# Kernel optimization log

Hardware: AMD Instinct MI355X
Metric: run time of the kernel (lower is better)

Reference implementation:

```python
import jax, jax.numpy as jnp
import numpy as np
from itertools import combinations

NDIM = 256
BATCH = 65536


def setup_inputs() -> dict:
    key = jax.random.key(0)
    k1, k2 = jax.random.split(key)
    pairs = np.array(list(combinations(range(NDIM), 2)), dtype=np.int32)  # [comb(ndim,2), 2]
    return {
        "x": jax.random.normal(k1, (BATCH, NDIM), dtype=jnp.float32),
        "rots": jax.random.normal(k2, (pairs.shape[0],), dtype=jnp.float32),
        "idx_i": jnp.asarray(pairs[:, 0]),
        "idx_j": jnp.asarray(pairs[:, 1]),
    }


def _build_mat(rots, idx_i, idx_j, ndim):
    # Equivalent to mat = R_last @ ... @ R_first @ I, then return mat.T.
    # Each Givens rotation R_(i,j,theta) only mixes rows i and j, so we update
    # two rows per step (O(ndim) work) instead of a dense ndim x ndim matmul.
    # Torch uses cfloat, but all imaginary parts are identically zero, so
    # float32 computes the same math.
    def step(mat, t):
        i, j, theta = t
        c = jnp.cos(theta)
        s = jnp.sin(theta)
        ri = mat[i]
        rj = mat[j]
        mat = mat.at[i].set(c * ri - s * rj)
        mat = mat.at[j].set(s * ri + c * rj)
        return mat, None

    mat0 = jnp.eye(ndim, dtype=rots.dtype)
    mat, _ = jax.lax.scan(step, mat0, (idx_i, idx_j, rots))
    return mat.T  # forward does x @ mat.T


def reference(x, rots, idx_i, idx_j):
    m = _build_mat(rots, idx_i, idx_j, x.shape[-1])  # [ndim, ndim]
    return x @ m
```

## Files before the change

### kernel.cpp

```cpp
#include <hip/hip_runtime.h>
#include <hip/hip_bf16.h>
#include <math.h>

#define NDIM 256
#define NROT 32640
#define NSEG 64
#define SEGLEN 510
#define MATE (NDIM * NDIM)
#define NODEE (2 * MATE)

typedef __bf16 bf16x4_t __attribute__((ext_vector_type(4)));
typedef __bf16 bf16x8_t __attribute__((ext_vector_type(8)));
typedef float f32x4_t __attribute__((ext_vector_type(4)));

__global__ __launch_bounds__(64, 1) void k_build(const float* __restrict__ rots,
                                                 __bf16* __restrict__ leaves) {
    __shared__ float tile[NDIM * 64];
    __shared__ float2 csl[SEGLEN + 8];
    const int t = threadIdx.x;
    const int seg = blockIdx.x >> 2;
    const int cg = blockIdx.x & 3;
    const int col = cg * 64 + t;

    const int kg0 = seg * SEGLEN;
    for (int u = t; u < SEGLEN; u += 64) {
        float th = rots[kg0 + u];
        float s, c;
        sincosf(th, &s, &c);
        csl[u] = make_float2(c, s);
    }
    for (int u = SEGLEN + t; u < SEGLEN + 8; u += 64) csl[u] = make_float2(1.f, 0.f);

    for (int r = 0; r < NDIM; r++) tile[r * 64 + t] = (r == col) ? 1.0f : 0.0f;

    int k = 0;
    int i = 0, cum = 0;
    while (cum + (NDIM - 1 - i) <= kg0) { cum += NDIM - 1 - i; i++; }
    int j = i + 1 + (kg0 - cum);

    while (k < SEGLEN) {
        float ri = tile[i * 64 + t];
        const int len = min(NDIM - j, SEGLEN - k);
        const int jend = j + len;
        const int nb = len >> 3;

        if (nb > 0) {
            float2 cv[8]; float rj[8];
            #pragma unroll
            for (int u = 0; u < 8; u++) cv[u] = csl[k + u];
            #pragma unroll
            for (int u = 0; u < 8; u++) rj[u] = tile[(j + u) * 64 + t];
            for (int b = 0; b < nb - 1; b++) {
                float2 cvn[8]; float rjn[8];
                #pragma unroll
                for (int u = 0; u < 8; u++) cvn[u] = csl[k + 8 + u];
                #pragma unroll
                for (int u = 0; u < 8; u++) rjn[u] = tile[(j + 8 + u) * 64 + t];
                #pragma unroll
                for (int u = 0; u < 8; u++) {
                    float nri = fmaf(cv[u].x, ri, -(cv[u].y * rj[u]));
                    rj[u]     = fmaf(cv[u].y, ri,  cv[u].x * rj[u]);
                    ri = nri;
                }
                #pragma unroll
                for (int u = 0; u < 8; u++) tile[(j + u) * 64 + t] = rj[u];
                #pragma unroll
                for (int u = 0; u < 8; u++) { cv[u] = cvn[u]; rj[u] = rjn[u]; }
                j += 8; k += 8;
            }
            #pragma unroll
            for (int u = 0; u < 8; u++) {
                float nri = fmaf(cv[u].x, ri, -(cv[u].y * rj[u]));
                rj[u]     = fmaf(cv[u].y, ri,  cv[u].x * rj[u]);
                ri = nri;
            }
            #pragma unroll
            for (int u = 0; u < 8; u++) tile[(j + u) * 64 + t] = rj[u];
            j += 8; k += 8;
        }
        for (; j < jend; j++, k++) {
            float2 cv = csl[k];
            float rj = tile[j * 64 + t];
            float nri = fmaf(cv.x, ri, -(cv.y * rj));
            tile[j * 64 + t] = fmaf(cv.y, ri, cv.x * rj);
            ri = nri;
        }
        tile[i * 64 + t] = ri;
        if (j == NDIM) { i++; j = i + 1; }
    }

    __bf16* hi = leaves + (size_t)seg * NODEE;
    __bf16* lo = hi + MATE;
    if (seg & 1) {
        for (int r = 0; r < NDIM; r++) {
            float v = tile[r * 64 + t];
            __bf16 h = (__bf16)v;
            hi[r * NDIM + col] = h;
            lo[r * NDIM + col] = (__bf16)(v - (float)h);
        }
    } else {
        for (int r0 = 0; r0 < NDIM; r0 += 8) {
            bf16x8_t vh, vl;
            #pragma unroll
            for (int u = 0; u < 8; u++) {
                float v = tile[(r0 + u) * 64 + t];
                __bf16 h = (__bf16)v;
                vh[u] = h;
                vl[u] = (__bf16)(v - (float)h);
            }
            *(bf16x8_t*)&hi[(size_t)col * NDIM + r0] = vh;
            *(bf16x8_t*)&lo[(size_t)col * NDIM + r0] = vl;
        }
    }
}

#define LDK 264
__global__ __launch_bounds__(256) void k_combine(const __bf16* __restrict__ src,
                                                 __bf16* __restrict__ dst,
                                                 int finalLevel) {
    __shared__ __bf16 planes[4][64 * LDK];

    const int p = blockIdx.x >> 4;
    const int qd = blockIdx.x & 15;
    const int rbq = (qd >> 2) * 64;
    const int cbq = (qd & 3) * 64;
    const __bf16* A = src + (size_t)(2 * p) * NODEE;
    const __bf16* B = src + (size_t)(2 * p + 1) * NODEE;
    __bf16* Chi = dst + (size_t)p * NODEE;
    __bf16* Clo = Chi + MATE;
    const bool storeT = (!finalLevel) && ((p & 1) == 0);

    const int t = threadIdx.x;
    const int wid = t >> 6, lane = t & 63;
    const int wr2 = (wid >> 1) * 32, wc2 = (wid & 1) * 32;
    const int lrow = lane & 15, kg = lane >> 4;

    const __bf16* plane_src[4] = {B, B + MATE, A, A + MATE};
    const int plane_row0[4] = {rbq, rbq, cbq, cbq};
    #pragma unroll
    for (int q = 0; q < 32; q++) {
        int g = q * 256 + t;
        int pl = g >> 11;
        int c = g & 2047;
        int row = c >> 5, sg = c & 31;
        bf16x8_t v = *(const bf16x8_t*)&plane_src[pl][(size_t)(plane_row0[pl] + row) * NDIM + sg * 8];
        *(bf16x8_t*)&planes[pl][row * LDK + sg * 8] = v;
    }
    __syncthreads();

    f32x4_t acc[2][2] = {};
    #pragma unroll
    for (int kc = 0; kc < 8; kc++) {
        bf16x8_t afh[2], afl[2], bfh[2], bfl[2];
        #pragma unroll
        for (int mt = 0; mt < 2; mt++) {
            int r = (wr2 + mt * 16 + lrow) * LDK + kc * 32 + kg * 8;
            afh[mt] = *(const bf16x8_t*)&planes[0][r];
            afl[mt] = *(const bf16x8_t*)&planes[1][r];
        }
        #pragma unroll
        for (int nt = 0; nt < 2; nt++) {
            int r = (wc2 + nt * 16 + lrow) * LDK + kc * 32 + kg * 8;
            bfh[nt] = *(const bf16x8_t*)&planes[2][r];
            bfl[nt] = *(const bf16x8_t*)&planes[3][r];
        }
        #pragma unroll
        for (int mt = 0; mt < 2; mt++)
            #pragma unroll
            for (int nt = 0; nt < 2; nt++) {
                acc[mt][nt] = __builtin_amdgcn_mfma_f32_16x16x32_bf16(afh[mt], bfh[nt], acc[mt][nt], 0, 0, 0);
                acc[mt][nt] = __builtin_amdgcn_mfma_f32_16x16x32_bf16(afh[mt], bfl[nt], acc[mt][nt], 0, 0, 0);
                acc[mt][nt] = __builtin_amdgcn_mfma_f32_16x16x32_bf16(afl[mt], bfh[nt], acc[mt][nt], 0, 0, 0);
            }
    }

    #pragma unroll
    for (int mt = 0; mt < 2; mt++)
        #pragma unroll
        for (int nt = 0; nt < 2; nt++) {
            int grow = rbq + wr2 + mt * 16 + kg * 4;
            int gcol = cbq + wc2 + nt * 16 + lrow;
            if (storeT) {
                bf16x4_t vh, vl;
                #pragma unroll
                for (int r = 0; r < 4; r++) {
                    float v = acc[mt][nt][r];
                    __bf16 h = (__bf16)v;
                    vh[r] = h;
                    vl[r] = (__bf16)(v - (float)h);
                }
                *(bf16x4_t*)&Chi[(size_t)gcol * NDIM + grow] = vh;
                *(bf16x4_t*)&Clo[(size_t)gcol * NDIM + grow] = vl;
            } else if (finalLevel) {
                #pragma unroll
                for (int r = 0; r < 4; r++)
                    Chi[(size_t)(grow + r) * NDIM + gcol] = (__bf16)acc[mt][nt][r];
            } else {
                #pragma unroll
                for (int r = 0; r < 4; r++) {
                    float v = acc[mt][nt][r];
                    __bf16 h = (__bf16)v;
                    Chi[(size_t)(grow + r) * NDIM + gcol] = h;
                    Clo[(size_t)(grow + r) * NDIM + gcol] = (__bf16)(v - (float)h);
                }
            }
        }
}

#define LDA 72
__global__ __launch_bounds__(256, 2) void k_gemm(const float* __restrict__ X,
                                                 const __bf16* __restrict__ Mhi,
                                                 float* __restrict__ Y) {
    __shared__ __bf16 As[128 * LDA];
    __shared__ __bf16 Bs[128 * LDA];
    const int bx = blockIdx.x;
    const int xcd = bx & 7;
    const int q = bx >> 3;
    const int bn = (q & 1) * 128;
    const int bm = (xcd + (q >> 1) * 8) * 128;
    const int t = threadIdx.x;
    const int wid = t >> 6;
    const int lane = t & 63;
    const int wr = (wid >> 1) * 64;
    const int wc = (wid & 1) * 64;
    const int lrow = lane & 15;
    const int kg = lane >> 4;

    f32x4_t acc[4][4] = {};

    f32x4_t ra[8];
    bf16x8_t rb[4];

    #pragma unroll
    for (int qq = 0; qq < 8; qq++) {
        int g = qq * 256 + t;
        ra[qq] = *(const f32x4_t*)&X[(size_t)(bm + (g >> 4)) * 256 + (g & 15) * 4];
    }
    #pragma unroll
    for (int qq = 0; qq < 4; qq++) {
        int g = qq * 256 + t;
        rb[qq] = *(const bf16x8_t*)&Mhi[(size_t)(bn + (g >> 3)) * 256 + (g & 7) * 8];
    }

    #pragma unroll
    for (int it = 0; it < 4; it++) {
        #pragma unroll
        for (int qq = 0; qq < 8; qq++) {
            int g = qq * 256 + t;
            f32x4_t v = ra[qq];
            bf16x4_t h = {(__bf16)v.x, (__bf16)v.y, (__bf16)v.z, (__bf16)v.w};
            *(bf16x4_t*)&As[(g >> 4) * LDA + (g & 15) * 4] = h;
        }
        #pragma unroll
        for (int qq = 0; qq < 4; qq++) {
            int g = qq * 256 + t;
            *(bf16x8_t*)&Bs[(g >> 3) * LDA + (g & 7) * 8] = rb[qq];
        }
        __syncthreads();

        if (it < 3) {
            int kc = (it + 1) * 64;
            #pragma unroll
            for (int qq = 0; qq < 8; qq++) {
                int g = qq * 256 + t;
                ra[qq] = *(const f32x4_t*)&X[(size_t)(bm + (g >> 4)) * 256 + kc + (g & 15) * 4];
            }
            #pragma unroll
            for (int qq = 0; qq < 4; qq++) {
                int g = qq * 256 + t;
                rb[qq] = *(const bf16x8_t*)&Mhi[(size_t)(bn + (g >> 3)) * 256 + kc + (g & 7) * 8];
            }
        }

        #pragma unroll
        for (int k2 = 0; k2 < 2; k2++) {
            bf16x8_t af[4], bfr[4];
            #pragma unroll
            for (int mt = 0; mt < 4; mt++)
                af[mt] = *(const bf16x8_t*)&As[(wr + mt * 16 + lrow) * LDA + k2 * 32 + kg * 8];
            #pragma unroll
            for (int nt = 0; nt < 4; nt++)
                bfr[nt] = *(const bf16x8_t*)&Bs[(wc + nt * 16 + lrow) * LDA + k2 * 32 + kg * 8];
            #pragma unroll
            for (int mt = 0; mt < 4; mt++)
                #pragma unroll
                for (int nt = 0; nt < 4; nt++)
                    acc[mt][nt] = __builtin_amdgcn_mfma_f32_16x16x32_bf16(af[mt], bfr[nt], acc[mt][nt], 0, 0, 0);
        }
        __syncthreads();
    }

    const int ocol = bn + wc + lrow;
    const int orow = bm + wr + kg * 4;
    #pragma unroll
    for (int mt = 0; mt < 4; mt++)
        #pragma unroll
        for (int nt = 0; nt < 4; nt++)
            #pragma unroll
            for (int r = 0; r < 4; r++)
                Y[(size_t)(orow + mt * 16 + r) * 256 + ocol + nt * 16] = acc[mt][nt][r];
}

extern "C" void kernel_launch(void* const* d_in, const int* in_sizes, int n_in,
                              void* d_out, int out_size, void* d_ws, size_t ws_size,
                              hipStream_t stream) {
    const float* x = (const float*)d_in[0];
    const float* rots = (const float*)d_in[1];
    float* out = (float*)d_out;

    __bf16* B0 = (__bf16*)d_ws;
    __bf16* B1 = B0 + (size_t)NSEG * NODEE;

    k_build<<<NSEG * 4, 64, 0, stream>>>(rots, B0);
    k_combine<<<32 * 16, 256, 0, stream>>>(B0, B1, 0);
    k_combine<<<16 * 16, 256, 0, stream>>>(B1, B0, 0);
    k_combine<<<8 * 16, 256, 0, stream>>>(B0, B1, 0);
    k_combine<<<4 * 16, 256, 0, stream>>>(B1, B0, 0);
    k_combine<<<2 * 16, 256, 0, stream>>>(B0, B1, 0);
    k_combine<<<1 * 16, 256, 0, stream>>>(B1, B0, 1);
    k_gemm<<<1024, 256, 0, stream>>>(x, B0, out);
}
```

Baseline: 227.4 us.

## Interleave build tile rows in groups of 8 for vectorized LDS access and double-buffer

Changes the shared-memory tile layout in the Givens build kernel from row-major [256][64] to [32][64][8], so each thread's eight consecutive rows are contiguous. This lets row updates use 128-bit LDS loads and stores. The inner rotation loop is restructured to process 16 rotations per step with A/B double-buffered register sets, plus peel and tail loops for unaligned starts. The aim is fewer LDS instructions and better latency hiding in the serial rotation chain. The cost is higher register pressure and more complex control flow.

```diff
diff --git a/kernel.cpp b/kernel.cpp
--- a/kernel.cpp
+++ b/kernel.cpp
@@ -13,103 +13,165 @@
 typedef __bf16 bf16x8_t __attribute__((ext_vector_type(8)));
 typedef float f32x4_t __attribute__((ext_vector_type(4)));
 
+
+#define ROT1(RJ, CS) { float nri_ = fmaf((CS).x, ri, -((CS).y * (RJ))); \
+                       (RJ) = fmaf((CS).y, ri, (CS).x * (RJ)); ri = nri_; }
+
+#define LOAD16(P, JB, KK) \
+    P##0 = *(const f32x4_t*)&tile[(JB)][t][0]; \
+    P##1 = *(const f32x4_t*)&tile[(JB)][t][4]; \
+    P##2 = *(const f32x4_t*)&tile[(JB) + 1][t][0]; \
+    P##3 = *(const f32x4_t*)&tile[(JB) + 1][t][4]; \
+    _Pragma("unroll") \
+    for (int u = 0; u < 16; u++) P##c[u] = csl[(KK) + u];
+
+#define COMP16(P, JB) \
+    _Pragma("unroll") \
+    for (int u = 0; u < 4; u++) ROT1(P##0[u], P##c[u]) \
+    _Pragma("unroll") \
+    for (int u = 0; u < 4; u++) ROT1(P##1[u], P##c[4 + u]) \
+    _Pragma("unroll") \
+    for (int u = 0; u < 4; u++) ROT1(P##2[u], P##c[8 + u]) \
+    _Pragma("unroll") \
+    for (int u = 0; u < 4; u++) ROT1(P##3[u], P##c[12 + u]) \
+    *(f32x4_t*)&tile[(JB)][t][0] = P##0; \
+    *(f32x4_t*)&tile[(JB)][t][4] = P##1; \
+    *(f32x4_t*)&tile[(JB) + 1][t][0] = P##2; \
+    *(f32x4_t*)&tile[(JB) + 1][t][4] = P##3;
+
 __global__ __launch_bounds__(64, 1) void k_build(const float* __restrict__ rots,
                                                  __bf16* __restrict__ leaves) {
-    __shared__ float tile[NDIM * 64];
-    __shared__ float2 csl[SEGLEN + 8];
+    __shared__ float tile[32][64][8];
+    __shared__ float2 csl[SEGLEN + 16];
     const int t = threadIdx.x;
     const int seg = blockIdx.x >> 2;
     const int cg = blockIdx.x & 3;
     const int col = cg * 64 + t;
-
     const int kg0 = seg * SEGLEN;
+
     for (int u = t; u < SEGLEN; u += 64) {
         float th = rots[kg0 + u];
         float s, c;
         sincosf(th, &s, &c);
         csl[u] = make_float2(c, s);
     }
-    for (int u = SEGLEN + t; u < SEGLEN + 8; u += 64) csl[u] = make_float2(1.f, 0.f);
-
-    for (int r = 0; r < NDIM; r++) tile[r * 64 + t] = (r == col) ? 1.0f : 0.0f;
+    for (int u = SEGLEN + t; u < SEGLEN + 16; u += 64) csl[u] = make_float2(1.f, 0.f);
+
+    #pragma unroll
+    for (int jb = 0; jb < 32; jb++) {
+        f32x4_t z0 = {0.f, 0.f, 0.f, 0.f}, z1 = {0.f, 0.f, 0.f, 0.f};
+        if ((col >> 3) == jb) {
+            if ((col & 7) < 4) z0[col & 3] = 1.0f;
+            else               z1[col & 3] = 1.0f;
+        }
+        *(f32x4_t*)&tile[jb][t][0] = z0;
+        *(f32x4_t*)&tile[jb][t][4] = z1;
+    }
 
     int k = 0;
     int i = 0, cum = 0;
     while (cum + (NDIM - 1 - i) <= kg0) { cum += NDIM - 1 - i; i++; }
     int j = i + 1 + (kg0 - cum);
 
+    float* T = &tile[0][0][0];
+    #define TADDR(r) ((((r) >> 3) * 512) + t * 8 + ((r) & 7))
+
     while (k < SEGLEN) {
-        float ri = tile[i * 64 + t];
-        const int len = min(NDIM - j, SEGLEN - k);
-        const int jend = j + len;
-        const int nb = len >> 3;
-
-        if (nb > 0) {
-            float2 cv[8]; float rj[8];
-            #pragma unroll
-            for (int u = 0; u < 8; u++) cv[u] = csl[k + u];
-            #pragma unroll
-            for (int u = 0; u < 8; u++) rj[u] = tile[(j + u) * 64 + t];
-            for (int b = 0; b < nb - 1; b++) {
-                float2 cvn[8]; float rjn[8];
-                #pragma unroll
-                for (int u = 0; u < 8; u++) cvn[u] = csl[k + 8 + u];
-                #pragma unroll
-                for (int u = 0; u < 8; u++) rjn[u] = tile[(j + 8 + u) * 64 + t];
-                #pragma unroll
-                for (int u = 0; u < 8; u++) {
-                    float nri = fmaf(cv[u].x, ri, -(cv[u].y * rj[u]));
-                    rj[u]     = fmaf(cv[u].y, ri,  cv[u].x * rj[u]);
-                    ri = nri;
-                }
-                #pragma unroll
-                for (int u = 0; u < 8; u++) tile[(j + u) * 64 + t] = rj[u];
-                #pragma unroll
-                for (int u = 0; u < 8; u++) { cv[u] = cvn[u]; rj[u] = rjn[u]; }
-                j += 8; k += 8;
-            }
-            #pragma unroll
-            for (int u = 0; u < 8; u++) {
-                float nri = fmaf(cv[u].x, ri, -(cv[u].y * rj[u]));
-                rj[u]     = fmaf(cv[u].y, ri,  cv[u].x * rj[u]);
-                ri = nri;
-            }
-            #pragma unroll
-            for (int u = 0; u < 8; u++) tile[(j + u) * 64 + t] = rj[u];
-            j += 8; k += 8;
-        }
-        for (; j < jend; j++, k++) {
-            float2 cv = csl[k];
-            float rj = tile[j * 64 + t];
-            float nri = fmaf(cv.x, ri, -(cv.y * rj));
-            tile[j * 64 + t] = fmaf(cv.y, ri, cv.x * rj);
-            ri = nri;
-        }
-        tile[i * 64 + t] = ri;
+        float ri = T[TADDR(i)];
+        int rem = min(NDIM - j, SEGLEN - k);
+
+        int npeel = min((8 - (j & 7)) & 7, rem);
+        for (int u = 0; u < npeel; u++) {
+            float2 cs = csl[k];
+            float rj = T[TADDR(j)];
+            float nri = fmaf(cs.x, ri, -(cs.y * rj));
+            T[TADDR(j)] = fmaf(cs.y, ri, cs.x * rj);
+            ri = nri; j++; k++;
+        }
+        rem -= npeel;
+
+        if (rem >= 16) {
+            int jb = j >> 3;
+            f32x4_t A0, A1, A2, A3, B0, B1, B2, B3;
+            float2 Ac[16], Bc[16];
+            LOAD16(A, jb, k)
+            while (rem >= 48) {
+                LOAD16(B, jb + 2, k + 16)
+                COMP16(A, jb)
+                jb += 2; j += 16; k += 16; rem -= 16;
+                LOAD16(A, jb + 2, k + 16)
+                COMP16(B, jb)
+                jb += 2; j += 16; k += 16; rem -= 16;
+            }
+            if (rem >= 32) {
+                LOAD16(B, jb + 2, k + 16)
+                COMP16(A, jb)
+                jb += 2; j += 16; k += 16; rem -= 16;
+                COMP16(B, jb)
+                jb += 2; j += 16; k += 16; rem -= 16;
+            } else {
+                COMP16(A, jb)
+                jb += 2; j += 16; k += 16; rem -= 16;
+            }
+        }
+
+        if (rem >= 8) {
+            int jb = j >> 3;
+            f32x4_t a0 = *(const f32x4_t*)&tile[jb][t][0];
+            f32x4_t a1 = *(const f32x4_t*)&tile[jb][t][4];
+            float2 cc[8];
+            #pragma unroll
+            for (int u = 0; u < 8; u++) cc[u] = csl[k + u];
+            #pragma unroll
+            for (int u = 0; u < 4; u++) ROT1(a0[u], cc[u])
+            #pragma unroll
+            for (int u = 0; u < 4; u++) ROT1(a1[u], cc[4 + u])
+            *(f32x4_t*)&tile[jb][t][0] = a0;
+            *(f32x4_t*)&tile[jb][t][4] = a1;
+            j += 8; k += 8; rem -= 8;
+        }
+
+        while (rem > 0) {
+            float2 cs = csl[k];
+            float rj = T[TADDR(j)];
+            float nri = fmaf(cs.x, ri, -(cs.y * rj));
+            T[TADDR(j)] = fmaf(cs.y, ri, cs.x * rj);
+            ri = nri; j++; k++; rem--;
+        }
+
+        T[TADDR(i)] = ri;
         if (j == NDIM) { i++; j = i + 1; }
     }
+    #undef TADDR
 
     __bf16* hi = leaves + (size_t)seg * NODEE;
     __bf16* lo = hi + MATE;
     if (seg & 1) {
-        for (int r = 0; r < NDIM; r++) {
-            float v = tile[r * 64 + t];
-            __bf16 h = (__bf16)v;
-            hi[r * NDIM + col] = h;
-            lo[r * NDIM + col] = (__bf16)(v - (float)h);
+        for (int jb = 0; jb < 32; jb++) {
+            f32x4_t v0 = *(const f32x4_t*)&tile[jb][t][0];
+            f32x4_t v1 = *(const f32x4_t*)&tile[jb][t][4];
+            #pragma unroll
+            for (int u = 0; u < 8; u++) {
+                float v = (u < 4) ? v0[u & 3] : v1[u & 3];
+                __bf16 h = (__bf16)v;
+                hi[(size_t)(jb * 8 + u) * NDIM + col] = h;
+                lo[(size_t)(jb * 8 + u) * NDIM + col] = (__bf16)(v - (float)h);
+            }
         }
     } else {
-        for (int r0 = 0; r0 < NDIM; r0 += 8) {
+        for (int jb = 0; jb < 32; jb++) {
+            f32x4_t v0 = *(const f32x4_t*)&tile[jb][t][0];
+            f32x4_t v1 = *(const f32x4_t*)&tile[jb][t][4];
             bf16x8_t vh, vl;
             #pragma unroll
             for (int u = 0; u < 8; u++) {
-                float v = tile[(r0 + u) * 64 + t];
+                float v = (u < 4) ? v0[u & 3] : v1[u & 3];
                 __bf16 h = (__bf16)v;
                 vh[u] = h;
                 vl[u] = (__bf16)(v - (float)h);
             }
-            *(bf16x8_t*)&hi[(size_t)col * NDIM + r0] = vh;
-            *(bf16x8_t*)&lo[(size_t)col * NDIM + r0] = vl;
+            *(bf16x8_t*)&hi[(size_t)col * NDIM + jb * 8] = vh;
+            *(bf16x8_t*)&lo[(size_t)col * NDIM + jb * 8] = vl;
         }
     }
 }
```

Result: faster. 222.5 us (-2.1%).
